# Performance work log

Hardware: AMD Instinct MI355X
Metric: run time of the kernel (lower is better)

Reference implementation:

```python
import jax, jax.numpy as jnp
import numpy as np

B, O, C, HID, H, W = 4, 8, 256, 128, 64, 64
STEPS = 2  # message passing steps


def _conv3x3(x, w, b):
    # x: [N,Cin,H,W], w: [Cout,Cin,3,3]
    y = jax.lax.conv_general_dilated(x, w, window_strides=(1, 1), padding='SAME',
                                     dimension_numbers=('NCHW', 'OIHW', 'NCHW'))
    return y + b[None, :, None, None]


def setup_inputs() -> dict:
    key = jax.random.key(0)
    ks = jax.random.split(key, 6)
    return {
        'batch_node_feats': jax.random.normal(ks[0], (B, C, H, W), jnp.float32),
        'batch_previous_masks': jax.random.uniform(ks[1], (B, O, H, W), jnp.float32),
        'batch_valid_indices': jnp.ones((B, O), jnp.bool_),
        'batch_previous_states': jnp.zeros((B, O), jnp.float32),  # unused (use_temporal_features=False)
        'enc_w': jax.random.normal(ks[2], (HID, C + 1, 3, 3), jnp.float32) * 0.02,
        'enc_b': jnp.zeros((HID,), jnp.float32),
        'gcn_w': jax.random.normal(ks[3], (HID, 2 * HID, 3, 3), jnp.float32) * 0.02,
        'gcn_b': jnp.zeros((HID,), jnp.float32),
        'ro_w': jax.random.normal(ks[4], (1, C + HID, 3, 3), jnp.float32) * 0.02,
        'ro_b': jnp.zeros((1,), jnp.float32),
    }


def reference(batch_node_feats, batch_previous_masks, batch_valid_indices,
              batch_previous_states, enc_w, enc_b, gcn_w, gcn_b, ro_w, ro_b):
    # All objects valid (batch_valid_indices all True) -> fully vectorized over B and O.
    feats = jnp.broadcast_to(batch_node_feats[:, None], (B, O, C, H, W))
    # Mask encoder: per-object state from frame feats + previous object mask.
    enc_in = jnp.concatenate([feats, batch_previous_masks[:, :, None]], axis=2)
    states = jax.nn.relu(_conv3x3(enc_in.reshape(B * O, C + 1, H, W), enc_w, enc_b))
    states = states.reshape(B, O, HID, H, W)
    # Fully-connected message passing: neighbors of i = all objects except i.
    for _ in range(STEPS):
        agg = states.sum(axis=1, keepdims=True) - states  # sum over others
        gcn_in = jnp.concatenate([states, agg], axis=2).reshape(B * O, 2 * HID, H, W)
        states = jax.nn.relu(_conv3x3(gcn_in, gcn_w, gcn_b)).reshape(B, O, HID, H, W)
    # Readout: per-object mask logits -> sigmoid.
    ro_in = jnp.concatenate([feats, states], axis=2).reshape(B * O, C + HID, H, W)
    out_masks = jax.nn.sigmoid(_conv3x3(ro_in, ro_w, ro_b)).reshape(B, O, H, W)
    return out_masks  # out_states is None when use_temporal_features=False
```

## Files before the change

kernel.cpp:

```cpp
#include <hip/hip_runtime.h>
#include <math.h>


typedef unsigned short ushort_t;
typedef _Float16 f16x8 __attribute__((ext_vector_type(8)));
typedef float f32x4 __attribute__((ext_vector_type(4)));

#define GLDS(gsrc, ldst)                                                      \
    __builtin_amdgcn_global_load_lds(                                         \
        (const __attribute__((address_space(1))) unsigned int*)(gsrc),        \
        (__attribute__((address_space(3))) unsigned int*)(ldst), 16, 0, 0)

__device__ __forceinline__ ushort_t f2h(float f) {
    _Float16 h = (_Float16)f;
    return *(ushort_t*)&h;
}
__device__ __forceinline__ float h2f(ushort_t u) {
    _Float16 h = *(_Float16*)&u;
    return (float)h;
}

__global__ __launch_bounds__(256) void prep_all(
    const float* __restrict__ feats, const float* __restrict__ enc_w,
    const float* __restrict__ gcn_w, const float* __restrict__ ro_w,
    ushort_t* __restrict__ featsT, ushort_t* __restrict__ WencF,
    ushort_t* __restrict__ WgcnS, ushort_t* __restrict__ WgcnD,
    ushort_t* __restrict__ WroQ, ushort_t* __restrict__ WroS)
{
    __shared__ float tile[64][65];
    int bid = blockIdx.x, t = threadIdx.x;
    if (bid < 1024) {
        int pt = bid & 63, ct = (bid >> 6) & 3, img = bid >> 8;
        int px_l = t & 63;
        const float* src = feats + ((size_t)img * 256 + ct * 64) * 4096 + pt * 64;
#pragma unroll
        for (int j = 0; j < 16; ++j) {
            int ci_l = (t >> 6) + j * 4;
            tile[px_l][ci_l] = src[(size_t)ci_l * 4096 + px_l];
        }
        __syncthreads();
        int px = t >> 2;
#pragma unroll
        for (int j = 0; j < 2; ++j) {
            int c8 = ((t & 3) + j * 4) * 8;
            uint4 v; ushort_t* pv = (ushort_t*)&v;
#pragma unroll
            for (int k = 0; k < 8; ++k) pv[k] = f2h(tile[px][c8 + k]);
            int cc = ct * 2 + (c8 >> 5);
            *(uint4*)(featsT + ((size_t)img * 8 + cc) * 131072 +
                      (size_t)(pt * 64 + px) * 32 + (c8 & 31)) = v;
        }
        return;
    }
    int i = (bid - 1024) * 256 + t;
    if (i < 294912) {
        int ci32 = i & 31, co = (i >> 5) & 127, tc = i >> 12;
        int tt = tc >> 3, cc = tc & 7, ci = cc * 32 + ci32;
        WencF[i] = f2h(enc_w[(co * 257 + ci) * 9 + tt]);
    } else if (i < 442368) {
        int j = i - 294912;
        int ci32 = j & 31, co = (j >> 5) & 127, tc = j >> 12;
        int tt = tc >> 2, cc = tc & 3, ci = cc * 32 + ci32;
        WgcnS[j] = f2h(gcn_w[(co * 256 + 128 + ci) * 9 + tt]);
    } else if (i < 589824) {
        int j = i - 442368;
        int ci32 = j & 31, co = (j >> 5) & 127, tc = j >> 12;
        int tt = tc >> 2, cc = tc & 3, ci = cc * 32 + ci32;
        WgcnD[j] = f2h(gcn_w[(co * 256 + ci) * 9 + tt] -
                       gcn_w[(co * 256 + 128 + ci) * 9 + tt]);
    } else if (i < 592128) {
        int j = i - 589824;
        int k = j & 7, r = j >> 3;
        int tt = r % 9, cq = r / 9, q = cq & 3, cc = cq >> 2;
        WroQ[j] = f2h(ro_w[(cc * 32 + q * 8 + k) * 9 + tt]);
    } else if (i < 593280) {
        int j = i - 592128;
        int k = j & 7, r = j >> 3;
        int tt = r % 9, cq = r / 9, q = cq & 3, cc = cq >> 2;
        WroS[j] = f2h(ro_w[(256 + cc * 32 + q * 8 + k) * 9 + tt]);
    }
}

template<int NCCBLK, bool FUSE>
__global__ __launch_bounds__(256, 3) void conv_k(
    const ushort_t* __restrict__ x, const ushort_t* __restrict__ W,
    ushort_t* __restrict__ out,
    const ushort_t* __restrict__ addp, const float* __restrict__ bias,
    int ncc_img)
{
    __shared__ ushort_t raw[25088];
    ushort_t* xs = raw;
    ushort_t* wlds = raw + 16896;
    ushort_t* eb16 = raw;

    const int rp = blockIdx.x, img = blockIdx.y, kz = blockIdx.z;
    const int row0 = rp * 2;
    const int cc0 = kz * NCCBLK;
    const int nchunk = 9 * NCCBLK;
    const int tid = threadIdx.x;
    const int w = tid >> 6, lane = tid & 63, lq = lane >> 4, lr = lane & 15;
    const int cg = w >> 1, pg = w & 1;

    const ushort_t* xb = x + (size_t)img * ncc_img * 131072;
    const int aoff0 = (cg * 64 + lr) * 32 + lq * 8;

    if (tid < 64) {
        int b = tid >> 5, r = (tid >> 3) & 3, c = (tid >> 2) & 1, s = tid & 3;
        *(uint4*)(xs + b * 8448 + r * 2112 + (c ? 65 : 0) * 32 + s * 8) =
            make_uint4(0, 0, 0, 0);
    }

    f32x4 acc[4][4];
#pragma unroll
    for (int a = 0; a < 4; ++a)
#pragma unroll
        for (int p = 0; p < 4; ++p) acc[a][p] = (f32x4){0.f, 0.f, 0.f, 0.f};

    const int gy = row0 - 1 + w;
    const bool row_ok = (unsigned)gy < 64u;
#define STAGE_ACT(cc_, buf_)                                                    \
    {                                                                           \
        ushort_t* dst = xs + (buf_) * 8448 + w * 2112 + 32;                     \
        if (row_ok) {                                                           \
            const ushort_t* src = xb + (size_t)(cc_) * 131072 + (size_t)gy * 2048; \
            GLDS(src + 0 * 512 + lane * 8, dst + 0 * 512);                      \
            GLDS(src + 1 * 512 + lane * 8, dst + 1 * 512);                      \
            GLDS(src + 2 * 512 + lane * 8, dst + 2 * 512);                      \
            GLDS(src + 3 * 512 + lane * 8, dst + 3 * 512);                      \
        } else {                                                                \
            *(uint4*)(dst + 0 * 512 + lane * 8) = make_uint4(0, 0, 0, 0);       \
            *(uint4*)(dst + 1 * 512 + lane * 8) = make_uint4(0, 0, 0, 0);       \
            *(uint4*)(dst + 2 * 512 + lane * 8) = make_uint4(0, 0, 0, 0);       \
            *(uint4*)(dst + 3 * 512 + lane * 8) = make_uint4(0, 0, 0, 0);       \
        }                                                                       \
    }
#define STAGE_W(t_, cc_, buf_)                                                  \
    {                                                                           \
        const ushort_t* src = W + ((size_t)((t_) * ncc_img + (cc_)) * 4096);    \
        ushort_t* dst = wlds + (buf_) * 4096;                                   \
        GLDS(src + (w * 2 + 0) * 512 + lane * 8, dst + (w * 2 + 0) * 512);      \
        GLDS(src + (w * 2 + 1) * 512 + lane * 8, dst + (w * 2 + 1) * 512);      \
    }

    STAGE_ACT(cc0, 0);
    STAGE_W(0, cc0, 0);

    int kc = 0;
#pragma unroll
    for (int ccl = 0; ccl < NCCBLK; ++ccl) {
        const int cc = cc0 + ccl;
        const int xbuf = ccl & 1;
#pragma unroll
        for (int t = 0; t < 9; ++t, ++kc) {
            __syncthreads();
            if (kc + 1 < nchunk) {
                if (t == 8) {
                    STAGE_W(0, cc + 1, (kc + 1) & 1);
                    STAGE_ACT(cc + 1, (ccl + 1) & 1);
                } else {
                    STAGE_W(t + 1, cc, (kc + 1) & 1);
                }
            }
            const int dy = t / 3, dx = t - 3 * dy;
            const ushort_t* wl = wlds + (kc & 1) * 4096 + aoff0;
            const ushort_t* xl = xs + xbuf * 8448 + (pg + dy) * 2112 + (dx + lr) * 32 + lq * 8;
            f16x8 A0 = *(const f16x8*)(wl);
            f16x8 A1 = *(const f16x8*)(wl + 512);
            f16x8 A2 = *(const f16x8*)(wl + 1024);
            f16x8 A3 = *(const f16x8*)(wl + 1536);
#pragma unroll
            for (int p = 0; p < 4; ++p) {
                f16x8 Bf = *(const f16x8*)(xl + p * 512);
                acc[0][p] = __builtin_amdgcn_mfma_f32_16x16x32_f16(A0, Bf, acc[0][p], 0, 0, 0);
                acc[1][p] = __builtin_amdgcn_mfma_f32_16x16x32_f16(A1, Bf, acc[1][p], 0, 0, 0);
                acc[2][p] = __builtin_amdgcn_mfma_f32_16x16x32_f16(A2, Bf, acc[2][p], 0, 0, 0);
                acc[3][p] = __builtin_amdgcn_mfma_f32_16x16x32_f16(A3, Bf, acc[3][p], 0, 0, 0);
            }
        }
    }

    ushort_t* obase = out + (size_t)(kz * gridDim.y + img) * 524288;
    const int b4 = img >> 3;
#pragma unroll
    for (int r = 0; r < 2; ++r) {
        __syncthreads();
        if (pg == r) {
#pragma unroll
            for (int cf = 0; cf < 4; ++cf)
#pragma unroll
                for (int pf = 0; pf < 4; ++pf) {
                    int px = pf * 16 + lr;
                    int co_l = cg * 64 + cf * 16 + lq * 4;
                    ushort_t pk[4];
#pragma unroll
                    for (int j = 0; j < 4; ++j) pk[j] = f2h(acc[cf][pf][j]);
                    *(uint2*)(eb16 + px * 136 + co_l) = *(uint2*)pk;
                }
        }
        __syncthreads();
#pragma unroll
        for (int k2 = 0; k2 < 4; ++k2) {
            int i = tid + k2 * 256;
            int px = i >> 4, c16 = i & 15;
            int pxg = (row0 + r) * 64 + px;
            size_t coff = (size_t)(c16 >> 2) * 131072 + (size_t)pxg * 32 + (c16 & 3) * 8;
            uint4 v = *(uint4*)(eb16 + px * 136 + c16 * 8);
            if constexpr (FUSE) {
                const ushort_t* vp = (const ushort_t*)&v;
                float vv[8];
#pragma unroll
                for (int k = 0; k < 8; ++k) vv[k] = h2f(vp[k]) + bias[c16 * 8 + k];
#pragma unroll
                for (int p = 0; p < 4; ++p) {
                    uint4 av = *(const uint4*)(addp + (size_t)(p * 4 + b4) * 524288 + coff);
                    const ushort_t* ap = (const ushort_t*)&av;
#pragma unroll
                    for (int k = 0; k < 8; ++k) vv[k] += h2f(ap[k]);
                }
                uint4 sv; ushort_t* sp = (ushort_t*)&sv;
#pragma unroll
                for (int k = 0; k < 8; ++k) sp[k] = f2h(fmaxf(vv[k], 0.f));
                *(uint4*)(obase + coff) = sv;
            } else {
                *(uint4*)(obase + coff) = v;
            }
        }
    }
#undef STAGE_ACT
#undef STAGE_W
}

__global__ __launch_bounds__(256) void sum8(const ushort_t* __restrict__ S,
                                            ushort_t* __restrict__ USum)
{
    int i = blockIdx.x * 256 + threadIdx.x;
    int s = i & 3, px = (i >> 2) & 4095, cc = (i >> 14) & 3, b = i >> 16;
    size_t coff = (size_t)cc * 131072 + (size_t)px * 32 + s * 8;
    const ushort_t* p = S + (size_t)b * 8 * 524288 + coff;
    float v[8] = {0, 0, 0, 0, 0, 0, 0, 0};
#pragma unroll
    for (int o = 0; o < 8; ++o) {
        uint4 xv = *(const uint4*)(p + (size_t)o * 524288);
        const ushort_t* xp = (const ushort_t*)&xv;
#pragma unroll
        for (int k = 0; k < 8; ++k) v[k] += h2f(xp[k]);
    }
    uint4 sv; ushort_t* sp = (ushort_t*)&sv;
#pragma unroll
    for (int k = 0; k < 8; ++k) sp[k] = f2h(v[k]);
    *(uint4*)(USum + (size_t)b * 524288 + coff) = sv;
}

__global__ __launch_bounds__(256) void enc_obj_sum(
    const float* __restrict__ masks, const float* __restrict__ enc_w,
    const float* __restrict__ enc_b, const ushort_t* __restrict__ U1p,
    ushort_t* __restrict__ S, ushort_t* __restrict__ USum)
{
    int i = blockIdx.x * 256 + threadIdx.x;
    int s = i & 3, px = (i >> 2) & 4095, cc = (i >> 14) & 3, b = i >> 16;
    int co = cc * 32 + s * 8;
    int y = px >> 6, xx = px & 63;
    size_t coff = (size_t)cc * 131072 + (size_t)px * 32 + s * 8;
    float base[8];
#pragma unroll
    for (int k = 0; k < 8; ++k) base[k] = enc_b[co + k];
#pragma unroll
    for (int p = 0; p < 8; ++p) {
        uint4 v = *(const uint4*)(U1p + (size_t)(p * 4 + b) * 524288 + coff);
        const ushort_t* vp = (const ushort_t*)&v;
#pragma unroll
        for (int k = 0; k < 8; ++k) base[k] += h2f(vp[k]);
    }
    float wm[8][9];
#pragma unroll
    for (int k = 0; k < 8; ++k) {
        const float* wp = enc_w + (size_t)((co + k) * 257 + 256) * 9;
#pragma unroll
        for (int t = 0; t < 9; ++t) wm[k][t] = wp[t];
    }
    float sacc[8] = {0, 0, 0, 0, 0, 0, 0, 0};
#pragma unroll
    for (int o = 0; o < 8; ++o) {
        const float* m = masks + (size_t)(b * 8 + o) * 4096;
        float mt[9];
#pragma unroll
        for (int dy = 0; dy < 3; ++dy)
#pragma unroll
            for (int dx = 0; dx < 3; ++dx) {
                int gy_ = y + dy - 1, gx = xx + dx - 1;
                mt[dy * 3 + dx] =
                    ((unsigned)gy_ < 64u && (unsigned)gx < 64u) ? m[gy_ * 64 + gx] : 0.f;
            }
        uint4 sv; ushort_t* sp = (ushort_t*)&sv;
#pragma unroll
        for (int k = 0; k < 8; ++k) {
            float acc = base[k];
#pragma unroll
            for (int t = 0; t < 9; ++t) acc = fmaf(mt[t], wm[k][t], acc);
            acc = fmaxf(acc, 0.f);
            sacc[k] += acc;
            sp[k] = f2h(acc);
        }
        *(uint4*)(S + (size_t)(b * 8 + o) * 524288 + coff) = sv;
    }
    uint4 sv; ushort_t* sp = (ushort_t*)&sv;
#pragma unroll
    for (int k = 0; k < 8; ++k) sp[k] = f2h(sacc[k]);
    *(uint4*)(USum + (size_t)b * 524288 + coff) = sv;
}

__global__ __launch_bounds__(256) void ro_shared(
    const ushort_t* __restrict__ featsT, const ushort_t* __restrict__ WroQ,
    float* __restrict__ YR)
{
    int i = blockIdx.x * 256 + threadIdx.x;
    int cu = i & 31, px = (i >> 5) & 4095, b = i >> 17;
    int cc = cu >> 2, q = cu & 3;
    int y = px >> 6, xcol = px & 63;
    const ushort_t* wp = WroQ + (size_t)(cc * 4 + q) * 72;
    float wreg[9][8];
#pragma unroll
    for (int t = 0; t < 9; ++t) {
        uint4 wv = *(const uint4*)(wp + t * 8);
        const ushort_t* wq = (const ushort_t*)&wv;
#pragma unroll
        for (int k = 0; k < 8; ++k) wreg[t][k] = h2f(wq[k]);
    }
    const ushort_t* fb = featsT + (size_t)(b * 8 + cc) * 131072 + q * 8;
    float acc = 0.f;
#pragma unroll
    for (int dy = 0; dy < 3; ++dy) {
        int gy = y + dy - 1;
        if ((unsigned)gy >= 64u) continue;
#pragma unroll
        for (int dx = 0; dx < 3; ++dx) {
            int gx = xcol + dx - 1;
            if ((unsigned)gx >= 64u) continue;
            uint4 v = *(const uint4*)(fb + (size_t)(gy * 64 + gx) * 32);
            const ushort_t* vp = (const ushort_t*)&v;
#pragma unroll
            for (int k = 0; k < 8; ++k)
                acc = fmaf(h2f(vp[k]), wreg[dy * 3 + dx][k], acc);
        }
    }
#pragma unroll
    for (int d = 16; d >= 1; d >>= 1) acc += __shfl_down(acc, d, 32);
    if (cu == 0) YR[b * 4096 + px] = acc;
}

__global__ __launch_bounds__(256) void ro_obj(
    const ushort_t* __restrict__ S, const ushort_t* __restrict__ WroS,
    const float* __restrict__ ro_b, const float* __restrict__ YR,
    float* __restrict__ out)
{
    int i = blockIdx.x * 256 + threadIdx.x;
    int cu = i & 15, px = (i >> 4) & 4095, n = i >> 16;
    int b = n >> 3;
    int cc = cu >> 2, q = cu & 3;
    int y = px >> 6, xcol = px & 63;
    const ushort_t* wp = WroS + (size_t)(cc * 4 + q) * 72;
    float wreg[9][8];
#pragma unroll
    for (int t = 0; t < 9; ++t) {
        uint4 wv = *(const uint4*)(wp + t * 8);
        const ushort_t* wq = (const ushort_t*)&wv;
#pragma unroll
        for (int k = 0; k < 8; ++k) wreg[t][k] = h2f(wq[k]);
    }
    const ushort_t* sb = S + ((size_t)n * 4 + cc) * 131072 + q * 8;
    float acc = 0.f;
#pragma unroll
    for (int dy = 0; dy < 3; ++dy) {
        int gy = y + dy - 1;
        if ((unsigned)gy >= 64u) continue;
#pragma unroll
        for (int dx = 0; dx < 3; ++dx) {
            int gx = xcol + dx - 1;
            if ((unsigned)gx >= 64u) continue;
            uint4 v = *(const uint4*)(sb + (size_t)(gy * 64 + gx) * 32);
            const ushort_t* vp = (const ushort_t*)&v;
#pragma unroll
            for (int k = 0; k < 8; ++k)
                acc = fmaf(h2f(vp[k]), wreg[dy * 3 + dx][k], acc);
        }
    }
#pragma unroll
    for (int d = 8; d >= 1; d >>= 1) acc += __shfl_down(acc, d, 16);
    if (cu == 0) {
        float v = acc + YR[b * 4096 + px] + ro_b[0];
        out[n * 4096 + px] = 1.f / (1.f + __expf(-v));
    }
}

extern "C" void kernel_launch(void* const* d_in, const int* in_sizes, int n_in,
                              void* d_out, int out_size, void* d_ws, size_t ws_size,
                              hipStream_t stream)
{
    const float* feats = (const float*)d_in[0];
    const float* masks = (const float*)d_in[1];
    const float* enc_w = (const float*)d_in[4];
    const float* enc_b = (const float*)d_in[5];
    const float* gcn_w = (const float*)d_in[6];
    const float* gcn_b = (const float*)d_in[7];
    const float* ro_w  = (const float*)d_in[8];
    const float* ro_b  = (const float*)d_in[9];
    float* out = (float*)d_out;

    ushort_t* WencF  = (ushort_t*)d_ws;
    ushort_t* WgcnS  = WencF + 294912;
    ushort_t* WgcnD  = WgcnS + 147456;
    ushort_t* WroQ   = WgcnD + 147456;
    ushort_t* WroS   = WroQ + 2304;
    ushort_t* featsT = WroS + 1152;
    ushort_t* Sa     = featsT + 4194304;
    ushort_t* Sb     = Sa + 16777216;
    ushort_t* USum   = Sb + 16777216;
    ushort_t* U1p16  = USum + 2097152;
    ushort_t* U2p16  = U1p16 + 16777216;
    float*    YR     = (float*)(U2p16 + 8388608);

    dim3 blk(256);

    prep_all<<<3344, blk, 0, stream>>>(feats, enc_w, gcn_w, ro_w,
                                       featsT, WencF, WgcnS, WgcnD, WroQ, WroS);

    conv_k<1, false><<<dim3(32, 4, 8), blk, 0, stream>>>(
        featsT, WencF, U1p16, nullptr, nullptr, 8);
    enc_obj_sum<<<1024, blk, 0, stream>>>(masks, enc_w, enc_b, U1p16, Sa, USum);

    conv_k<1, false><<<dim3(32, 4, 4), blk, 0, stream>>>(
        USum, WgcnS, U2p16, nullptr, nullptr, 4);
    conv_k<4, true><<<dim3(32, 32, 1), blk, 0, stream>>>(
        Sa, WgcnD, Sb, U2p16, gcn_b, 4);
    sum8<<<1024, blk, 0, stream>>>(Sb, USum);

    conv_k<1, false><<<dim3(32, 4, 4), blk, 0, stream>>>(
        USum, WgcnS, U2p16, nullptr, nullptr, 4);
    conv_k<4, true><<<dim3(32, 32, 1), blk, 0, stream>>>(
        Sb, WgcnD, Sa, U2p16, gcn_b, 4);

    ro_shared<<<2048, blk, 0, stream>>>(featsT, WroQ, YR);
    ro_obj<<<8192, blk, 0, stream>>>(Sa, WroS, ro_b, YR, out);
}
```

Before: 272.9 us.

## Fuse object-sum into conv staging, merge readout-shared into encoder kernel, halve encoder splits

Removes the separate sum8 kernel. The second-step gcn conv now sums the 8 object states directly while staging activations into LDS, using vector f16 adds instead of async global-to-LDS loads. The ro_shared work is folded into the encoder-epilogue kernel as extra blocks, and the first encoder conv uses 2 channel chunks per block so it writes 4 partials instead of 8. This cuts launches and one intermediate round trip. In exchange, staging in the summing conv becomes synchronous and reads 8x more data, and the sum is accumulated in f16 rather than f32.

```diff
diff --git a/kernel.cpp b/kernel.cpp
--- a/kernel.cpp
+++ b/kernel.cpp
@@ -81,7 +81,7 @@
     }
 }
 
-template<int NCCBLK, bool FUSE>
+template<int NCCBLK, bool FUSE, bool SUMIN>
 __global__ __launch_bounds__(256, 3) void conv_k(
     const ushort_t* __restrict__ x, const ushort_t* __restrict__ W,
     ushort_t* __restrict__ out,
@@ -101,7 +101,9 @@
     const int w = tid >> 6, lane = tid & 63, lq = lane >> 4, lr = lane & 15;
     const int cg = w >> 1, pg = w & 1;
 
-    const ushort_t* xb = x + (size_t)img * ncc_img * 131072;
+    const size_t objstride = (size_t)ncc_img * 131072;
+    const ushort_t* xb = SUMIN ? x + (size_t)img * 8 * objstride
+                               : x + (size_t)img * objstride;
     const int aoff0 = (cg * 64 + lr) * 32 + lq * 8;
 
     if (tid < 64) {
@@ -123,10 +125,22 @@
         ushort_t* dst = xs + (buf_) * 8448 + w * 2112 + 32;                     \
         if (row_ok) {                                                           \
             const ushort_t* src = xb + (size_t)(cc_) * 131072 + (size_t)gy * 2048; \
-            GLDS(src + 0 * 512 + lane * 8, dst + 0 * 512);                      \
-            GLDS(src + 1 * 512 + lane * 8, dst + 1 * 512);                      \
-            GLDS(src + 2 * 512 + lane * 8, dst + 2 * 512);                      \
-            GLDS(src + 3 * 512 + lane * 8, dst + 3 * 512);                      \
+            if constexpr (SUMIN) {                                              \
+                _Pragma("unroll")                                               \
+                for (int u_ = 0; u_ < 4; ++u_) {                                \
+                    f16x8 a_ = {0, 0, 0, 0, 0, 0, 0, 0};                        \
+                    _Pragma("unroll")                                           \
+                    for (int o_ = 0; o_ < 8; ++o_)                              \
+                        a_ = a_ + *(const f16x8*)(src + (size_t)o_ * objstride + \
+                                                  u_ * 512 + lane * 8);         \
+                    *(f16x8*)(dst + u_ * 512 + lane * 8) = a_;                  \
+                }                                                               \
+            } else {                                                            \
+                GLDS(src + 0 * 512 + lane * 8, dst + 0 * 512);                  \
+                GLDS(src + 1 * 512 + lane * 8, dst + 1 * 512);                  \
+                GLDS(src + 2 * 512 + lane * 8, dst + 2 * 512);                  \
+                GLDS(src + 3 * 512 + lane * 8, dst + 3 * 512);                  \
+            }                                                                   \
         } else {                                                                \
             *(uint4*)(dst + 0 * 512 + lane * 8) = make_uint4(0, 0, 0, 0);       \
             *(uint4*)(dst + 1 * 512 + lane * 8) = make_uint4(0, 0, 0, 0);       \
@@ -230,33 +244,51 @@
 #undef STAGE_W
 }
 
-__global__ __launch_bounds__(256) void sum8(const ushort_t* __restrict__ S,
-                                            ushort_t* __restrict__ USum)
-{
-    int i = blockIdx.x * 256 + threadIdx.x;
-    int s = i & 3, px = (i >> 2) & 4095, cc = (i >> 14) & 3, b = i >> 16;
-    size_t coff = (size_t)cc * 131072 + (size_t)px * 32 + s * 8;
-    const ushort_t* p = S + (size_t)b * 8 * 524288 + coff;
-    float v[8] = {0, 0, 0, 0, 0, 0, 0, 0};
-#pragma unroll
-    for (int o = 0; o < 8; ++o) {
-        uint4 xv = *(const uint4*)(p + (size_t)o * 524288);
-        const ushort_t* xp = (const ushort_t*)&xv;
-#pragma unroll
-        for (int k = 0; k < 8; ++k) v[k] += h2f(xp[k]);
-    }
-    uint4 sv; ushort_t* sp = (ushort_t*)&sv;
-#pragma unroll
-    for (int k = 0; k < 8; ++k) sp[k] = f2h(v[k]);
-    *(uint4*)(USum + (size_t)b * 524288 + coff) = sv;
-}
-
-__global__ __launch_bounds__(256) void enc_obj_sum(
+__global__ __launch_bounds__(256) void enc_obj_ro(
     const float* __restrict__ masks, const float* __restrict__ enc_w,
     const float* __restrict__ enc_b, const ushort_t* __restrict__ U1p,
-    ushort_t* __restrict__ S, ushort_t* __restrict__ USum)
+    const ushort_t* __restrict__ featsT, const ushort_t* __restrict__ WroQ,
+    ushort_t* __restrict__ S, ushort_t* __restrict__ USum,
+    float* __restrict__ YR)
 {
-    int i = blockIdx.x * 256 + threadIdx.x;
+    int bid = blockIdx.x, tid = threadIdx.x;
+    if (bid >= 1024) {
+        int i = (bid - 1024) * 256 + tid;
+        int cu = i & 31, px = (i >> 5) & 4095, b = i >> 17;
+        int cc = cu >> 2, q = cu & 3;
+        int y = px >> 6, xcol = px & 63;
+        const ushort_t* wp = WroQ + (size_t)(cc * 4 + q) * 72;
+        float wreg[9][8];
+#pragma unroll
+        for (int t = 0; t < 9; ++t) {
+            uint4 wv = *(const uint4*)(wp + t * 8);
+            const ushort_t* wq = (const ushort_t*)&wv;
+#pragma unroll
+            for (int k = 0; k < 8; ++k) wreg[t][k] = h2f(wq[k]);
+        }
+        const ushort_t* fb = featsT + (size_t)(b * 8 + cc) * 131072 + q * 8;
+        float acc = 0.f;
+#pragma unroll
+        for (int dy = 0; dy < 3; ++dy) {
+            int gy = y + dy - 1;
+            if ((unsigned)gy >= 64u) continue;
+#pragma unroll
+            for (int dx = 0; dx < 3; ++dx) {
+                int gx = xcol + dx - 1;
+                if ((unsigned)gx >= 64u) continue;
+                uint4 v = *(const uint4*)(fb + (size_t)(gy * 64 + gx) * 32);
+                const ushort_t* vp = (const ushort_t*)&v;
+#pragma unroll
+                for (int k = 0; k < 8; ++k)
+                    acc = fmaf(h2f(vp[k]), wreg[dy * 3 + dx][k], acc);
+            }
+        }
+#pragma unroll
+        for (int d = 16; d >= 1; d >>= 1) acc += __shfl_down(acc, d, 32);
+        if (cu == 0) YR[b * 4096 + px] = acc;
+        return;
+    }
+    int i = bid * 256 + tid;
     int s = i & 3, px = (i >> 2) & 4095, cc = (i >> 14) & 3, b = i >> 16;
     int co = cc * 32 + s * 8;
     int y = px >> 6, xx = px & 63;
@@ -265,7 +297,7 @@
 #pragma unroll
     for (int k = 0; k < 8; ++k) base[k] = enc_b[co + k];
 #pragma unroll
-    for (int p = 0; p < 8; ++p) {
+    for (int p = 0; p < 4; ++p) {
         uint4 v = *(const uint4*)(U1p + (size_t)(p * 4 + b) * 524288 + coff);
         const ushort_t* vp = (const ushort_t*)&v;
 #pragma unroll
@@ -307,45 +339,6 @@
 #pragma unroll
     for (int k = 0; k < 8; ++k) sp[k] = f2h(sacc[k]);
     *(uint4*)(USum + (size_t)b * 524288 + coff) = sv;
-}
-
-__global__ __launch_bounds__(256) void ro_shared(
-    const ushort_t* __restrict__ featsT, const ushort_t* __restrict__ WroQ,
-    float* __restrict__ YR)
-{
-    int i = blockIdx.x * 256 + threadIdx.x;
-    int cu = i & 31, px = (i >> 5) & 4095, b = i >> 17;
-    int cc = cu >> 2, q = cu & 3;
-    int y = px >> 6, xcol = px & 63;
-    const ushort_t* wp = WroQ + (size_t)(cc * 4 + q) * 72;
-    float wreg[9][8];
-#pragma unroll
-    for (int t = 0; t < 9; ++t) {
-        uint4 wv = *(const uint4*)(wp + t * 8);
-        const ushort_t* wq = (const ushort_t*)&wv;
-#pragma unroll
-        for (int k = 0; k < 8; ++k) wreg[t][k] = h2f(wq[k]);
-    }
-    const ushort_t* fb = featsT + (size_t)(b * 8 + cc) * 131072 + q * 8;
-    float acc = 0.f;
-#pragma unroll
-    for (int dy = 0; dy < 3; ++dy) {
-        int gy = y + dy - 1;
-        if ((unsigned)gy >= 64u) continue;
-#pragma unroll
-        for (int dx = 0; dx < 3; ++dx) {
-            int gx = xcol + dx - 1;
-            if ((unsigned)gx >= 64u) continue;
-            uint4 v = *(const uint4*)(fb + (size_t)(gy * 64 + gx) * 32);
-            const ushort_t* vp = (const ushort_t*)&v;
-#pragma unroll
-            for (int k = 0; k < 8; ++k)
-                acc = fmaf(h2f(vp[k]), wreg[dy * 3 + dx][k], acc);
-        }
-    }
-#pragma unroll
-    for (int d = 16; d >= 1; d >>= 1) acc += __shfl_down(acc, d, 32);
-    if (cu == 0) YR[b * 4096 + px] = acc;
 }
 
 __global__ __launch_bounds__(256) void ro_obj(
@@ -416,7 +409,7 @@
     ushort_t* Sb     = Sa + 16777216;
     ushort_t* USum   = Sb + 16777216;
     ushort_t* U1p16  = USum + 2097152;
-    ushort_t* U2p16  = U1p16 + 16777216;
+    ushort_t* U2p16  = U1p16 + 8388608;
     float*    YR     = (float*)(U2p16 + 8388608);
 
     dim3 blk(256);
@@ -424,21 +417,20 @@
     prep_all<<<3344, blk, 0, stream>>>(feats, enc_w, gcn_w, ro_w,
                                        featsT, WencF, WgcnS, WgcnD, WroQ, WroS);
 
-    conv_k<1, false><<<dim3(32, 4, 8), blk, 0, stream>>>(
+    conv_k<2, false, false><<<dim3(32, 4, 4), blk, 0, stream>>>(
         featsT, WencF, U1p16, nullptr, nullptr, 8);
-    enc_obj_sum<<<1024, blk, 0, stream>>>(masks, enc_w, enc_b, U1p16, Sa, USum);
-
-    conv_k<1, false><<<dim3(32, 4, 4), blk, 0, stream>>>(
+    enc_obj_ro<<<3072, blk, 0, stream>>>(masks, enc_w, enc_b, U1p16,
+                                         featsT, WroQ, Sa, USum, YR);
+
+    conv_k<1, false, false><<<dim3(32, 4, 4), blk, 0, stream>>>(
         USum, WgcnS, U2p16, nullptr, nullptr, 4);
-    conv_k<4, true><<<dim3(32, 32, 1), blk, 0, stream>>>(
+    conv_k<4, true, false><<<dim3(32, 32, 1), blk, 0, stream>>>(
         Sa, WgcnD, Sb, U2p16, gcn_b, 4);
-    sum8<<<1024, blk, 0, stream>>>(Sb, USum);
-
-    conv_k<1, false><<<dim3(32, 4, 4), blk, 0, stream>>>(
-        USum, WgcnS, U2p16, nullptr, nullptr, 4);
-    conv_k<4, true><<<dim3(32, 32, 1), blk, 0, stream>>>(
+
+    conv_k<1, false, true><<<dim3(32, 4, 4), blk, 0, stream>>>(
+        Sb, WgcnS, U2p16, nullptr, nullptr, 4);
+    conv_k<4, true, false><<<dim3(32, 32, 1), blk, 0, stream>>>(
         Sb, WgcnD, Sa, U2p16, gcn_b, 4);
 
-    ro_shared<<<2048, blk, 0, stream>>>(featsT, WroQ, YR);
     ro_obj<<<8192, blk, 0, stream>>>(Sa, WroS, ro_b, YR, out);
 }
```

Result: no change. 269.7 us (-1.2%).
